# Optimization experiments

Measured on AMD Instinct MI355X. Metric: run time of the kernel, lower is better.

## Reference

```python
import jax, jax.numpy as jnp
import numpy as np

N = 100000   # nodes
E = 1600000  # directed edges
B = 512      # graphs in batch
F = 9        # atom feature columns (OGB AtomEncoder)
V = 128      # vocab per atom feature
H = 256      # nhid
C = 10       # num_classes


def setup_inputs() -> dict:
    key = jax.random.key(0)
    ks = jax.random.split(key, 14)
    s = lambda k, shape: (jax.random.normal(k, shape, jnp.float32) * 0.05)
    return {
        "x": jax.random.randint(ks[0], (N, F), 0, V),
        "edge_index": jax.random.randint(ks[1], (2, E), 0, N),
        "batch": jnp.sort(jax.random.randint(ks[2], (N,), 0, B)),
        "atom_emb": s(ks[3], (F, V, H)),
        "W1": s(ks[4], (H, H)), "b1": s(ks[5], (H,)),
        "W2": s(ks[6], (H, H)), "b2": s(ks[7], (H,)),
        "W3": s(ks[8], (H, H)), "b3": s(ks[9], (H,)),
        "cw1": s(ks[10], (H, H // 2)), "cb1": s(ks[11], (H // 2,)),
        "cw2": s(ks[12], (H // 2, C)), "cb2": s(ks[13], (C,)),
    }


def reference(x, edge_index, batch, atom_emb, W1, b1, W2, b2, W3, b3, cw1, cb1, cw2, cb2):
    n = x.shape[0]
    # AtomEncoder: sum of per-column embeddings -> [N, H]
    h = atom_emb[jnp.arange(F)[None, :], x].sum(axis=1)

    # GCN normalization with self-loops (PyG GCNConv default)
    loop = jnp.arange(n, dtype=edge_index.dtype)
    row = jnp.concatenate([edge_index[0], loop])  # source
    col = jnp.concatenate([edge_index[1], loop])  # target
    deg = jax.ops.segment_sum(jnp.ones_like(col, jnp.float32), col, num_segments=n)
    dis = deg ** -0.5  # deg >= 1 because of self-loops
    norm = dis[row] * dis[col]  # [E+N]

    def gcn(feat, W, b):
        m = feat @ W                                   # [N, H]
        agg = jax.ops.segment_sum(norm[:, None] * m[row], col, num_segments=n)
        return agg + b

    x1 = jax.nn.relu(gcn(h, W1, b1))
    x2 = jax.nn.relu(gcn(x1, W2, b2))
    x3 = jax.nn.relu(gcn(x2, W3, b3))

    # global mean pool per graph, summed across the three layers
    counts = jax.ops.segment_sum(jnp.ones((n,), jnp.float32), batch, num_segments=B)
    pooled = jax.ops.segment_sum(x1 + x2 + x3, batch, num_segments=B) / counts[:, None]

    # classifier (dropout is identity in eval mode)
    hdn = jax.nn.relu(pooled @ cw1 + cb1)
    out = hdn @ cw2 + cb2
    return (out, 0)
```

## Files before the change

kernel.cpp:

```cpp
#include <hip/hip_runtime.h>
#include <hip/hip_bf16.h>
#include <cstdint>

#define HDIM 256
#define H2   128

using f32x4  = __attribute__((ext_vector_type(4))) float;
using bf16x8 = __attribute__((ext_vector_type(8))) short;
using u16x8  = __attribute__((ext_vector_type(8))) unsigned short;

__device__ inline unsigned short f2bf(float f) {
    unsigned x = __builtin_bit_cast(unsigned, f);
    return (unsigned short)((x + 0x7fffu + ((x >> 16) & 1u)) >> 16);
}
__device__ inline float bf2f(unsigned short u) {
    unsigned x = ((unsigned)u) << 16;
    return __builtin_bit_cast(float, x);
}

__global__ void k_deg(const int* __restrict__ col, int* __restrict__ deg0, int e) {
    int i = blockIdx.x * blockDim.x + threadIdx.x;
    if (i < e) atomicAdd(&deg0[col[i]], 1);
}

__global__ void k_scan1(const int* __restrict__ deg0, int* __restrict__ ptr,
                        int* __restrict__ bsum, int n) {
    __shared__ int sd[256];
    int i = blockIdx.x * 256 + threadIdx.x;
    int v = (i < n) ? deg0[i] : 0;
    sd[threadIdx.x] = v;
    __syncthreads();
    for (int off = 1; off < 256; off <<= 1) {
        int t = (threadIdx.x >= off) ? sd[threadIdx.x - off] : 0;
        __syncthreads();
        sd[threadIdx.x] += t;
        __syncthreads();
    }
    if (i < n) ptr[i] = sd[threadIdx.x] - v;
    if (threadIdx.x == 255) bsum[blockIdx.x] = sd[255];
}

__global__ void k_scan2(int* __restrict__ bsum, int nb) {
    __shared__ int sd[512];
    int t = threadIdx.x;
    int v = (t < nb) ? bsum[t] : 0;
    sd[t] = v;
    __syncthreads();
    for (int off = 1; off < 512; off <<= 1) {
        int x = (t >= off) ? sd[t - off] : 0;
        __syncthreads();
        sd[t] += x;
        __syncthreads();
    }
    if (t < nb) bsum[t] = sd[t] - v;
}

__global__ void k_scan3(int* __restrict__ ptr, const int* __restrict__ bsum,
                        const int* __restrict__ deg0, float* __restrict__ dis, int n) {
    int i = blockIdx.x * 256 + threadIdx.x;
    if (i < n) {
        ptr[i] += bsum[blockIdx.x];
        dis[i] = rsqrtf((float)deg0[i] + 1.0f);
    }
}

__global__ __launch_bounds__(256) void k_fill8(const int* __restrict__ row,
                                               const int* __restrict__ col,
                                               const int* __restrict__ ptr,
                                               int* __restrict__ cursor,
                                               int* __restrict__ csr, int e) {
    int xcd   = blockIdx.x & 7;
    int chunk = blockIdx.x >> 3;
    int base  = chunk * 2048;
    int end   = base + 2048; if (end > e) end = e;
    for (int i = base + threadIdx.x; i < end; i += 256) {
        int c = col[i];
        if (((c >> 3) & 7) == xcd) {
            int s = atomicAdd(&cursor[c], 1);
            csr[ptr[c] + s] = row[i];
        }
    }
}

__global__ void k_emb(const float* __restrict__ emb, short* __restrict__ embb, int tot) {
    int i = blockIdx.x * 256 + threadIdx.x;
    if (i < tot) embb[i] = (short)f2bf(emb[i]);
}

__global__ __launch_bounds__(256) void k_atom(const int* __restrict__ x,
                                              const short* __restrict__ embb,
                                              short* __restrict__ h,
                                              int n, int F, int V) {
    int node = blockIdx.x * 4 + (threadIdx.x >> 6);
    int lane = threadIdx.x & 63;
    if (node >= n) return;
    int xv = x[node * F + (lane < F ? lane : 0)];
    float acc[4] = {};
    for (int f = 0; f < F; ++f) {
        int idx = __shfl(xv, f, 64);
        ushort4 v = *(const ushort4*)((const unsigned short*)embb +
                                      ((size_t)(f * V + idx)) * HDIM + lane * 4);
        acc[0] += bf2f(v.x); acc[1] += bf2f(v.y);
        acc[2] += bf2f(v.z); acc[3] += bf2f(v.w);
    }
    ushort4 o = { f2bf(acc[0]), f2bf(acc[1]), f2bf(acc[2]), f2bf(acc[3]) };
    *(ushort4*)(h + (size_t)node * HDIM + lane * 4) = o;
}

__global__ void k_wt3(const float* __restrict__ W1, const float* __restrict__ W2,
                      const float* __restrict__ W3, short* __restrict__ Wt1,
                      short* __restrict__ Wt2, short* __restrict__ Wt3) {
    const float* W = (blockIdx.y == 0) ? W1 : (blockIdx.y == 1) ? W2 : W3;
    short* Wt      = (blockIdx.y == 0) ? Wt1 : (blockIdx.y == 1) ? Wt2 : Wt3;
    int i = blockIdx.x * 256 + threadIdx.x;
    int nn = i >> 8, k = i & 255;
    Wt[nn * HDIM + k] = (short)f2bf(W[k * HDIM + nn]);
}

__global__ __launch_bounds__(256, 4) void k_gemm(const short* __restrict__ A,
                                                 const short* __restrict__ Wt,
                                                 short* __restrict__ Co, int n) {
    __shared__ unsigned char As[64 * 512];
    int row0 = blockIdx.x * 64;
    int t = threadIdx.x;
    int wid  = t >> 6;
    int lane = t & 63;
#pragma unroll
    for (int j = 0; j < 8; ++j) {
        int c  = (wid * 8 + j) * 64 + lane;
        int r  = c >> 5;
        int cb = (c & 31) * 16;
        int gr = row0 + r; if (gr >= n) gr = n - 1;
        const unsigned int* g = (const unsigned int*)
            ((const char*)A + (size_t)gr * 512 + (cb ^ ((r & 7) << 4)));
        unsigned int* l = (unsigned int*)(As + (size_t)(wid * 8 + j) * 1024);
        __builtin_amdgcn_global_load_lds(g, l, 16, 0, 0);
    }
    __syncthreads();

    int lm = lane & 15;
    int kg = lane >> 4;
    int colw = wid * 64;
    f32x4 acc[4][4] = {};
#pragma unroll 2
    for (int kk = 0; kk < 8; ++kk) {
        bf16x8 a[4], b[4];
#pragma unroll
        for (int i = 0; i < 4; ++i) {
            int R = i * 16 + lm;
            int boff = (kk * 64 + kg * 16) ^ ((R & 7) << 4);
            a[i] = *(const bf16x8*)(As + R * 512 + boff);
        }
#pragma unroll
        for (int j = 0; j < 4; ++j) {
            int cidx = colw + j * 16 + lm;
            b[j] = *(const bf16x8*)(Wt + (size_t)cidx * HDIM + kk * 32 + kg * 8);
        }
#pragma unroll
        for (int i = 0; i < 4; ++i)
#pragma unroll
            for (int j = 0; j < 4; ++j)
                acc[i][j] = __builtin_amdgcn_mfma_f32_16x16x32_bf16(a[i], b[j], acc[i][j], 0, 0, 0);
    }
#pragma unroll
    for (int i = 0; i < 4; ++i)
#pragma unroll
        for (int j = 0; j < 4; ++j) {
            int c = colw + j * 16 + lm;
#pragma unroll
            for (int r4 = 0; r4 < 4; ++r4) {
                int r = row0 + i * 16 + kg * 4 + r4;
                if (r < n) Co[(size_t)r * HDIM + c] = (short)f2bf(acc[i][j][r4]);
            }
        }
}

__global__ __launch_bounds__(256) void k_agg(const short* __restrict__ mS,
                                             const int* __restrict__ csr_src,
                                             const int* __restrict__ ptr,
                                             const int* __restrict__ deg0,
                                             const float* __restrict__ dis,
                                             const float* __restrict__ bias,
                                             short* __restrict__ xout, int n) {
    int node = blockIdx.x * 4 + (threadIdx.x >> 6);
    if (node >= n) return;
    int lane = threadIdx.x & 63;
    int half = lane >> 5;
    int cl = lane & 31;
    const unsigned short* m = (const unsigned short*)mS;
    float dv = dis[node];
    float acc[8] = {};
    if (half == 0) {
        u16x8 r = *(const u16x8*)(m + (size_t)node * HDIM + cl * 8);
        float sw = dv * dv;
#pragma unroll
        for (int j = 0; j < 8; ++j) acc[j] = sw * bf2f(r[j]);
    }
    int start = ptr[node];
    int cnt = deg0[node];
    for (int base = 0; base < cnt; base += 64) {
        int mm = cnt - base; if (mm > 64) mm = 64;
        int uu = 0; float du = 0.f;
        if (lane < mm) {
            uu = __builtin_nontemporal_load(&csr_src[start + base + lane]);
            du = dis[uu];
        }
        int nst = (mm + 7) >> 3;
        for (int s = 0; s < nst; ++s) {
            u16x8 r[4]; float w[4];
#pragma unroll
            for (int q = 0; q < 4; ++q) {
                int i = 8 * s + 2 * q + half;
                int u   = __shfl(uu, i & 63, 64);
                float ww = dv * __shfl(du, i & 63, 64);
                bool v = i < mm;
                w[q] = v ? ww : 0.f;
                r[q] = *(const u16x8*)(m + (size_t)(v ? u : 0) * HDIM + cl * 8);
            }
#pragma unroll
            for (int q = 0; q < 4; ++q)
#pragma unroll
                for (int j = 0; j < 8; ++j) acc[j] += w[q] * bf2f(r[q][j]);
        }
    }
#pragma unroll
    for (int j = 0; j < 8; ++j) acc[j] += __shfl_xor(acc[j], 32, 64);
    if (half == 0) {
        const float4 b0 = *(const float4*)(bias + cl * 8);
        const float4 b1 = *(const float4*)(bias + cl * 8 + 4);
        float bb[8] = {b0.x, b0.y, b0.z, b0.w, b1.x, b1.y, b1.z, b1.w};
        u16x8 o;
#pragma unroll
        for (int j = 0; j < 8; ++j)
            o[j] = f2bf(fmaxf(acc[j] + bb[j], 0.f));
        *(u16x8*)((unsigned short*)xout + (size_t)node * HDIM + cl * 8) = o;
    }
}

__global__ __launch_bounds__(256) void k_pool(const short* __restrict__ x1,
                                              const short* __restrict__ x2,
                                              const short* __restrict__ x3,
                                              const int* __restrict__ batch,
                                              float* __restrict__ partial,
                                              int n, int B) {
    __shared__ float spool[8][HDIM];
    int g = blockIdx.x, seg = blockIdx.y, t = threadIdx.x;
    int cg = t & 31, rl = t >> 5;
    auto lb = [&](int key) {
        int lo = 0, hi = n;
        while (lo < hi) { int mid = (lo + hi) >> 1; if (batch[mid] < key) lo = mid + 1; else hi = mid; }
        return lo;
    };
    int lo = lb(g), hi = lb(g + 1);
    int len = hi - lo;
    int per = (len + 3) >> 2;
    int s0 = lo + seg * per;
    int s1 = s0 + per; if (s1 > hi) s1 = hi;
    float acc[8] = {};
    for (int r = s0 + rl; r < s1; r += 8) {
        size_t base = (size_t)r * HDIM + cg * 8;
        u16x8 a = *(const u16x8*)((const unsigned short*)x1 + base);
        u16x8 b = *(const u16x8*)((const unsigned short*)x2 + base);
        u16x8 c = *(const u16x8*)((const unsigned short*)x3 + base);
#pragma unroll
        for (int j = 0; j < 8; ++j)
            acc[j] += bf2f(a[j]) + bf2f(b[j]) + bf2f(c[j]);
    }
#pragma unroll
    for (int j = 0; j < 8; ++j) spool[rl][cg * 8 + j] = acc[j];
    __syncthreads();
    float s = 0.f;
#pragma unroll
    for (int r2 = 0; r2 < 8; ++r2) s += spool[r2][t];
    partial[(size_t)(seg * B + g) * HDIM + t] = s;
}

__global__ __launch_bounds__(256) void k_cls(const float* __restrict__ partial,
                                             const int* __restrict__ batch,
                                             const float* __restrict__ cw1,
                                             const float* __restrict__ cb1,
                                             const float* __restrict__ cw2,
                                             const float* __restrict__ cb2,
                                             float* __restrict__ out,
                                             int n, int B, int C) {
    __shared__ float sp[HDIM];
    __shared__ float sh[H2];
    int g = blockIdx.x, t = threadIdx.x;
    auto lb = [&](int key) {
        int lo = 0, hi = n;
        while (lo < hi) { int mid = (lo + hi) >> 1; if (batch[mid] < key) lo = mid + 1; else hi = mid; }
        return lo;
    };
    int lo = lb(g), hi = lb(g + 1);
    int cnt = hi - lo; if (cnt < 1) cnt = 1;
    float s = 0.f;
#pragma unroll
    for (int seg = 0; seg < 4; ++seg)
        s += partial[(size_t)(seg * B + g) * HDIM + t];
    sp[t] = s / (float)cnt;
    __syncthreads();
    if (t < H2) {
        float a = cb1[t];
        for (int h = 0; h < HDIM; ++h) a += sp[h] * cw1[h * H2 + t];
        sh[t] = fmaxf(a, 0.f);
    }
    __syncthreads();
    if (t < C) {
        float o = cb2[t];
        for (int j = 0; j < H2; ++j) o += sh[j] * cw2[j * C + t];
        out[g * C + t] = o;
    }
    if (g == 0 && t == 0) out[B * C] = 0.f;
}

extern "C" void kernel_launch(void* const* d_in, const int* in_sizes, int n_in,
                              void* d_out, int out_size, void* d_ws, size_t ws_size,
                              hipStream_t stream) {
    const int* x      = (const int*)d_in[0];
    const int* erow   = (const int*)d_in[1];
    const int* batch  = (const int*)d_in[2];
    const float* emb  = (const float*)d_in[3];
    const float* W1   = (const float*)d_in[4];
    const float* b1   = (const float*)d_in[5];
    const float* W2   = (const float*)d_in[6];
    const float* b2   = (const float*)d_in[7];
    const float* W3   = (const float*)d_in[8];
    const float* b3   = (const float*)d_in[9];
    const float* cw1  = (const float*)d_in[10];
    const float* cb1  = (const float*)d_in[11];
    const float* cw2  = (const float*)d_in[12];
    const float* cb2  = (const float*)d_in[13];
    float* out = (float*)d_out;

    const int N = in_sizes[2];
    const int E = in_sizes[1] / 2;
    const int F = in_sizes[0] / N;
    const int V = in_sizes[3] / (F * HDIM);
    const int C = in_sizes[13];
    const int B = (out_size - 1) / C;
    const int* ecol = erow + E;
    const int EMBTOT = F * V * HDIM;

    char* w = (char*)d_ws;
    auto carve = [&](size_t bytes) {
        void* p = (void*)w;
        w += (bytes + 255) & ~(size_t)255;
        return p;
    };
    short* P0     = (short*)carve((size_t)N * HDIM * 2);
    short* P1     = (short*)carve((size_t)N * HDIM * 2);
    short* P2     = (short*)carve((size_t)N * HDIM * 2);
    short* mS     = (short*)carve((size_t)N * HDIM * 2);
    short* embb   = (short*)carve((size_t)EMBTOT * 2);
    short* Wt1    = (short*)carve((size_t)HDIM * HDIM * 2);
    short* Wt2    = (short*)carve((size_t)HDIM * HDIM * 2);
    short* Wt3    = (short*)carve((size_t)HDIM * HDIM * 2);
    float* partial= (float*)carve((size_t)4 * B * HDIM * 4);
    float* dis    = (float*)carve((size_t)N * 4);
    int* deg0     = (int*)carve((size_t)N * 4);
    int* ptr      = (int*)carve((size_t)N * 4);
    int* cursor   = (int*)carve((size_t)N * 4);
    int* bsum     = (int*)carve(1024 * 4);
    int* csr      = (int*)carve((size_t)E * 4);

    int nblk = (N + 255) / 256;

    hipMemsetAsync(deg0, 0, (size_t)N * 4, stream);
    hipMemsetAsync(cursor, 0, (size_t)N * 4, stream);
    k_deg<<<(E + 255) / 256, 256, 0, stream>>>(ecol, deg0, E);
    k_scan1<<<nblk, 256, 0, stream>>>(deg0, ptr, bsum, N);
    k_scan2<<<1, 512, 0, stream>>>(bsum, nblk);
    k_scan3<<<nblk, 256, 0, stream>>>(ptr, bsum, deg0, dis, N);
    int nch = (E + 2047) / 2048;
    k_fill8<<<nch * 8, 256, 0, stream>>>(erow, ecol, ptr, cursor, csr, E);
    k_emb<<<(EMBTOT + 255) / 256, 256, 0, stream>>>(emb, embb, EMBTOT);
    dim3 wgrid(HDIM, 3);
    k_wt3<<<wgrid, 256, 0, stream>>>(W1, W2, W3, Wt1, Wt2, Wt3);
    k_atom<<<(N + 3) / 4, 256, 0, stream>>>(x, embb, P0, N, F, V);

    int ggrid = (N + 63) / 64;
    int agrid = (N + 3) / 4;

    k_gemm<<<ggrid, 256, 0, stream>>>(P0, Wt1, mS, N);
    k_agg<<<agrid, 256, 0, stream>>>(mS, csr, ptr, deg0, dis, b1, P1, N);
    k_gemm<<<ggrid, 256, 0, stream>>>(P1, Wt2, mS, N);
    k_agg<<<agrid, 256, 0, stream>>>(mS, csr, ptr, deg0, dis, b2, P2, N);
    k_gemm<<<ggrid, 256, 0, stream>>>(P2, Wt3, mS, N);
    k_agg<<<agrid, 256, 0, stream>>>(mS, csr, ptr, deg0, dis, b3, P0, N);

    dim3 pgrid(B, 4);
    k_pool<<<pgrid, 256, 0, stream>>>(P1, P2, P0, batch, partial, N, B);
    k_cls<<<B, 256, 0, stream>>>(partial, batch, cw1, cb1, cw2, cb2, out, N, B, C);
}
```

Baseline: 726.7 us.

## Partition degree atomics by XCD, merge prep kernels, split GEMM A-tile load into halves

The degree-count kernel now uses the same XCD-partitioned chunk scheme as the CSR fill, so each XCD's atomics hit a disjoint slice of destination nodes and stay in its local L2. The weight-transpose and embedding bf16 conversion kernels are merged into one launch to save a launch. The GEMM loads its A tile as two K-halves and waits only for the first half before starting MFMAs, overlapping the second half's load with compute. The cost is redundant reads of the column array by eight block groups, plus hand-placed waitcnt and barrier instructions that depend on the exact order in which loads are issued.

New measurement: 730.2 us. About the same (+0.5%).

```diff
diff --git a/kernel.cpp b/kernel.cpp
--- a/kernel.cpp
+++ b/kernel.cpp
@@ -18,9 +18,16 @@
     return __builtin_bit_cast(float, x);
 }
 
-__global__ void k_deg(const int* __restrict__ col, int* __restrict__ deg0, int e) {
-    int i = blockIdx.x * blockDim.x + threadIdx.x;
-    if (i < e) atomicAdd(&deg0[col[i]], 1);
+__global__ __launch_bounds__(256) void k_deg8(const int* __restrict__ col,
+                                              int* __restrict__ deg0, int e) {
+    int xcd   = blockIdx.x & 7;
+    int chunk = blockIdx.x >> 3;
+    int base  = chunk * 2048;
+    int end   = base + 2048; if (end > e) end = e;
+    for (int i = base + threadIdx.x; i < end; i += 256) {
+        int c = col[i];
+        if (((c >> 3) & 7) == xcd) atomicAdd(&deg0[c], 1);
+    }
 }
 
 __global__ void k_scan1(const int* __restrict__ deg0, int* __restrict__ ptr,
@@ -82,9 +89,23 @@
     }
 }
 
-__global__ void k_emb(const float* __restrict__ emb, short* __restrict__ embb, int tot) {
-    int i = blockIdx.x * 256 + threadIdx.x;
-    if (i < tot) embb[i] = (short)f2bf(emb[i]);
+__global__ void k_prep(const float* __restrict__ W1, const float* __restrict__ W2,
+                       const float* __restrict__ W3, short* __restrict__ Wt1,
+                       short* __restrict__ Wt2, short* __restrict__ Wt3,
+                       const float* __restrict__ emb, short* __restrict__ embb,
+                       int embtot) {
+    int b = blockIdx.x;
+    if (b < 768) {
+        int layer = b >> 8;
+        const float* W = (layer == 0) ? W1 : (layer == 1) ? W2 : W3;
+        short* Wt      = (layer == 0) ? Wt1 : (layer == 1) ? Wt2 : Wt3;
+        int i = (b & 255) * 256 + threadIdx.x;
+        int nn = i >> 8, k = i & 255;
+        Wt[nn * HDIM + k] = (short)f2bf(W[k * HDIM + nn]);
+    } else {
+        int i = (b - 768) * 256 + threadIdx.x;
+        if (i < embtot) embb[i] = (short)f2bf(emb[i]);
+    }
 }
 
 __global__ __launch_bounds__(256) void k_atom(const int* __restrict__ x,
@@ -107,49 +128,51 @@
     *(ushort4*)(h + (size_t)node * HDIM + lane * 4) = o;
 }
 
-__global__ void k_wt3(const float* __restrict__ W1, const float* __restrict__ W2,
-                      const float* __restrict__ W3, short* __restrict__ Wt1,
-                      short* __restrict__ Wt2, short* __restrict__ Wt3) {
-    const float* W = (blockIdx.y == 0) ? W1 : (blockIdx.y == 1) ? W2 : W3;
-    short* Wt      = (blockIdx.y == 0) ? Wt1 : (blockIdx.y == 1) ? Wt2 : Wt3;
-    int i = blockIdx.x * 256 + threadIdx.x;
-    int nn = i >> 8, k = i & 255;
-    Wt[nn * HDIM + k] = (short)f2bf(W[k * HDIM + nn]);
-}
-
 __global__ __launch_bounds__(256, 4) void k_gemm(const short* __restrict__ A,
                                                  const short* __restrict__ Wt,
                                                  short* __restrict__ Co, int n) {
-    __shared__ unsigned char As[64 * 512];
+    __shared__ unsigned char As[2 * 64 * 256];
     int row0 = blockIdx.x * 64;
     int t = threadIdx.x;
     int wid  = t >> 6;
     int lane = t & 63;
 #pragma unroll
-    for (int j = 0; j < 8; ++j) {
-        int c  = (wid * 8 + j) * 64 + lane;
-        int r  = c >> 5;
-        int cb = (c & 31) * 16;
-        int gr = row0 + r; if (gr >= n) gr = n - 1;
-        const unsigned int* g = (const unsigned int*)
-            ((const char*)A + (size_t)gr * 512 + (cb ^ ((r & 7) << 4)));
-        unsigned int* l = (unsigned int*)(As + (size_t)(wid * 8 + j) * 1024);
-        __builtin_amdgcn_global_load_lds(g, l, 16, 0, 0);
-    }
-    __syncthreads();
+    for (int p = 0; p < 2; ++p)
+#pragma unroll
+        for (int jj = 0; jj < 4; ++jj) {
+            int ci = (wid * 4 + jj) * 64 + lane;
+            int r  = ci >> 4;
+            int kb = (ci & 15) * 16;
+            int gr = row0 + r; if (gr >= n) gr = n - 1;
+            const unsigned int* g = (const unsigned int*)
+                ((const char*)A + (size_t)gr * 512 + p * 256 + (kb ^ ((r & 7) << 4)));
+            unsigned int* l = (unsigned int*)(As + p * 16384 + (size_t)(wid * 4 + jj) * 1024);
+            __builtin_amdgcn_global_load_lds(g, l, 16, 0, 0);
+        }
 
     int lm = lane & 15;
     int kg = lane >> 4;
     int colw = wid * 64;
     f32x4 acc[4][4] = {};
-#pragma unroll 2
+
+    asm volatile("s_waitcnt vmcnt(4)" ::: "memory");
+    __builtin_amdgcn_s_barrier();
+    __builtin_amdgcn_sched_barrier(0);
+
+#pragma unroll
     for (int kk = 0; kk < 8; ++kk) {
+        if (kk == 4) {
+            asm volatile("s_waitcnt vmcnt(0)" ::: "memory");
+            __builtin_amdgcn_s_barrier();
+            __builtin_amdgcn_sched_barrier(0);
+        }
+        int p = kk >> 2;
         bf16x8 a[4], b[4];
 #pragma unroll
         for (int i = 0; i < 4; ++i) {
             int R = i * 16 + lm;
-            int boff = (kk * 64 + kg * 16) ^ ((R & 7) << 4);
-            a[i] = *(const bf16x8*)(As + R * 512 + boff);
+            int boff = ((kk & 3) * 64 + kg * 16) ^ ((R & 7) << 4);
+            a[i] = *(const bf16x8*)(As + p * 16384 + R * 256 + boff);
         }
 #pragma unroll
         for (int j = 0; j < 4; ++j) {
@@ -364,18 +387,17 @@
     int* csr      = (int*)carve((size_t)E * 4);
 
     int nblk = (N + 255) / 256;
+    int nch = (E + 2047) / 2048;
 
     hipMemsetAsync(deg0, 0, (size_t)N * 4, stream);
     hipMemsetAsync(cursor, 0, (size_t)N * 4, stream);
-    k_deg<<<(E + 255) / 256, 256, 0, stream>>>(ecol, deg0, E);
+    k_deg8<<<nch * 8, 256, 0, stream>>>(ecol, deg0, E);
     k_scan1<<<nblk, 256, 0, stream>>>(deg0, ptr, bsum, N);
     k_scan2<<<1, 512, 0, stream>>>(bsum, nblk);
     k_scan3<<<nblk, 256, 0, stream>>>(ptr, bsum, deg0, dis, N);
-    int nch = (E + 2047) / 2048;
     k_fill8<<<nch * 8, 256, 0, stream>>>(erow, ecol, ptr, cursor, csr, E);
-    k_emb<<<(EMBTOT + 255) / 256, 256, 0, stream>>>(emb, embb, EMBTOT);
-    dim3 wgrid(HDIM, 3);
-    k_wt3<<<wgrid, 256, 0, stream>>>(W1, W2, W3, Wt1, Wt2, Wt3);
+    int prep_blocks = 768 + (EMBTOT + 255) / 256;
+    k_prep<<<prep_blocks, 256, 0, stream>>>(W1, W2, W3, Wt1, Wt2, Wt3, emb, embb, EMBTOT);
     k_atom<<<(N + 3) / 4, 256, 0, stream>>>(x, embb, P0, N, F, V);
 
     int ggrid = (N + 63) / 64;
```
